# Performance work log

Measured on AMD Instinct MI355X. Metric: run time of the kernel, lower is better.

Reference implementation:

```python
import jax, jax.numpy as jnp
import numpy as np

B, S, CL, DIM, HEADS, FFN = 2, 2048, 512, 2048, 16, 8192
EPS = 1e-6


def rms_norm(x, w):
    return x * jax.lax.rsqrt(jnp.mean(x * x, axis=-1, keepdims=True) + EPS) * w


def mha(q, k, v, num_heads):
    b, sq, d = q.shape
    sk = k.shape[1]
    hd = d // num_heads
    q = q.reshape(b, sq, num_heads, hd)
    k = k.reshape(b, sk, num_heads, hd)
    v = v.reshape(b, sk, num_heads, hd)
    attn = jnp.einsum('bqhd,bkhd->bhqk', q, k) * (hd ** -0.5)
    attn = jax.nn.softmax(attn, axis=-1)
    out = jnp.einsum('bhqk,bkhd->bqhd', attn, v)
    return out.reshape(b, sq, d)


def setup_inputs() -> dict:
    key = jax.random.key(0)
    ks = iter(jax.random.split(key, 48))
    nrm = lambda shape, scale: jax.random.normal(next(ks), shape, jnp.float32) * scale
    w_scale = DIM ** -0.5
    inp = {
        'x': nrm((B, S, DIM), 1.0),
        'e': nrm((B, 6, DIM), 0.5),
        'context': nrm((B, CL, DIM), 1.0),
        'modulation': nrm((1, 6, DIM), w_scale),
        'norm1_w': jnp.ones((DIM,), jnp.float32),
        'norm2_w': jnp.ones((DIM,), jnp.float32),
        'norm3_w': jnp.ones((DIM,), jnp.float32),
        'sa_nq_w': jnp.ones((DIM,), jnp.float32),
        'sa_nk_w': jnp.ones((DIM,), jnp.float32),
        'ffn_norm_w': jnp.ones((DIM,), jnp.float32),
        'sa_qw': nrm((DIM, DIM), w_scale), 'sa_qb': jnp.zeros((DIM,), jnp.float32),
        'sa_kw': nrm((DIM, DIM), w_scale), 'sa_kb': jnp.zeros((DIM,), jnp.float32),
        'sa_vw': nrm((DIM, DIM), w_scale), 'sa_vb': jnp.zeros((DIM,), jnp.float32),
        'sa_ow': nrm((DIM, DIM), w_scale), 'sa_ob': jnp.zeros((DIM,), jnp.float32),
        'ca_qw': nrm((DIM, DIM), w_scale), 'ca_qb': jnp.zeros((DIM,), jnp.float32),
        'ca_kw': nrm((DIM, DIM), w_scale), 'ca_kb': jnp.zeros((DIM,), jnp.float32),
        'ca_vw': nrm((DIM, DIM), w_scale), 'ca_vb': jnp.zeros((DIM,), jnp.float32),
        'ca_ow': nrm((DIM, DIM), w_scale), 'ca_ob': jnp.zeros((DIM,), jnp.float32),
        'ffn_w1': nrm((DIM, FFN), w_scale), 'ffn_b1': jnp.zeros((FFN,), jnp.float32),
        'ffn_w2': nrm((FFN, DIM), FFN ** -0.5), 'ffn_b2': jnp.zeros((DIM,), jnp.float32),
    }
    return inp


def reference(x, e, context, modulation, norm1_w, norm2_w, norm3_w, sa_nq_w, sa_nk_w,
              ffn_norm_w, sa_qw, sa_qb, sa_kw, sa_kb, sa_vw, sa_vb, sa_ow, sa_ob,
              ca_qw, ca_qb, ca_kw, ca_kb, ca_vw, ca_vb, ca_ow, ca_ob,
              ffn_w1, ffn_b1, ffn_w2, ffn_b2):
    # AdaLN modulation: (modulation + e) chunked into 6 along dim=1 -> each [B,1,DIM]
    mod = modulation + e
    e0, e1, e2, e3, e4, e5 = [mod[:, i:i + 1, :] for i in range(6)]

    # --- self attention with qk_norm=True ---
    h = rms_norm(x, norm1_w) * (1.0 + e1) + e0
    q = rms_norm(h @ sa_qw + sa_qb, sa_nq_w)
    k = rms_norm(h @ sa_kw + sa_kb, sa_nk_w)
    v = h @ sa_vw + sa_vb
    y = mha(q, k, v, HEADS) @ sa_ow + sa_ob
    x = x + y * e2

    # --- cross attention (cross_attn_norm=False, no qk norm) ---
    h = rms_norm(x, norm2_w)
    q = h @ ca_qw + ca_qb
    k = context @ ca_kw + ca_kb
    v = context @ ca_vw + ca_vb
    y = mha(q, k, v, HEADS) @ ca_ow + ca_ob
    x = x + y

    # --- FFN: modulate(norm3(x)) -> RMSNorm -> Linear -> GELU(tanh) -> Linear ---
    h = rms_norm(x, norm3_w) * (1.0 + e4) + e3
    h = rms_norm(h, ffn_norm_w)
    h = jax.nn.gelu(h @ ffn_w1 + ffn_b1, approximate=True)
    y = h @ ffn_w2 + ffn_b2
    x = x + y * e5
    return x
```

## Files before the change

### kernel.cpp

```cpp
#include <hip/hip_runtime.h>
#include <hip/hip_bf16.h>
#include <cstdint>

#define DIM   2048
#define HEADS 16
#define HD    128
#define SEQ   2048
#define CLEN  512
#define FFND  8192
#define BATCH 2

using bf16 = __hip_bfloat16;
typedef __attribute__((ext_vector_type(8))) short  short8;
typedef __attribute__((ext_vector_type(4))) short  short4v;
typedef __attribute__((ext_vector_type(4))) float  f32x4;
typedef __attribute__((ext_vector_type(8))) __bf16 bf16x8;

__device__ __forceinline__ short f2bs(float f){ bf16 h = __float2bfloat16(f); return __builtin_bit_cast(short, h); }
__device__ __forceinline__ float bs2f(short s){ return __builtin_bit_cast(float, (uint32_t)((uint16_t)s) << 16); }

__device__ __forceinline__ f32x4 mfma16(short8 a, short8 b, f32x4 c){
  return __builtin_amdgcn_mfma_f32_16x16x32_bf16(
      __builtin_bit_cast(bf16x8, a), __builtin_bit_cast(bf16x8, b), c, 0, 0, 0);
}

__device__ __forceinline__ void gload_lds16(const void* g, const void* l){
  __builtin_amdgcn_global_load_lds(
      (const __attribute__((address_space(1))) void*)(uintptr_t)g,
      (__attribute__((address_space(3))) void*)(uint32_t)(uintptr_t)l, 16, 0, 0);
}

__device__ __forceinline__ float block_sum(float v, float* sbuf, int tid){
  #pragma unroll
  for (int m = 32; m >= 1; m >>= 1) v += __shfl_xor(v, m, 64);
  const int w = tid >> 6;
  if ((tid & 63) == 0) sbuf[w] = v;
  __syncthreads();
  float r = sbuf[0] + sbuf[1] + sbuf[2] + sbuf[3];
  __syncthreads();
  return r;
}


__global__ void modadd_k(const float* __restrict__ m, const float* __restrict__ e,
                         float* __restrict__ out){
  int i = blockIdx.x * 256 + threadIdx.x;
  out[i] = m[i % (6 * DIM)] + e[i];
}

__global__ void f2b8_k(const float* __restrict__ in, bf16* __restrict__ out){
  int i = blockIdx.x * 256 + threadIdx.x;
  const float4* p = (const float4*)in;
  float4 a = p[2*i], c = p[2*i+1];
  short8 o;
  o[0]=f2bs(a.x); o[1]=f2bs(a.y); o[2]=f2bs(a.z); o[3]=f2bs(a.w);
  o[4]=f2bs(c.x); o[5]=f2bs(c.y); o[6]=f2bs(c.z); o[7]=f2bs(c.w);
  *((short8*)out + i) = o;
}

__global__ __launch_bounds__(256) void transpose_w(const float* __restrict__ W,
                                                   bf16* __restrict__ Wt, int K, int N){
  __shared__ float tile[32][33];
  const int tx = threadIdx.x & 31, ty = threadIdx.x >> 5;
  const size_t k0 = blockIdx.y * 32, n0 = blockIdx.x * 32;
  #pragma unroll
  for (int i = 0; i < 4; i++)
    tile[ty + i*8][tx] = W[(k0 + ty + i*8) * (size_t)N + n0 + tx];
  __syncthreads();
  #pragma unroll
  for (int i = 0; i < 4; i++)
    Wt[(n0 + ty + i*8) * (size_t)K + k0 + tx] = __float2bfloat16(tile[tx][ty + i*8]);
}

template<int MODE>
__global__ __launch_bounds__(256) void norm_x(const float* __restrict__ x,
    const float* __restrict__ w1, const float* __restrict__ w2,
    const float* __restrict__ mod, bf16* __restrict__ out, int S)
{
  const int row = blockIdx.x, tid = threadIdx.x;
  const int b = row / S;
  __shared__ float sbuf[4];
  const float* xr = x + (size_t)row * DIM;
  float v[8];
  #pragma unroll
  for (int i = 0; i < 2; i++){
    float4 t = *(const float4*)(xr + i*1024 + tid*4);
    v[i*4+0]=t.x; v[i*4+1]=t.y; v[i*4+2]=t.z; v[i*4+3]=t.w;
  }
  float ss = 0.f;
  #pragma unroll
  for (int j = 0; j < 8; j++) ss += v[j]*v[j];
  ss = block_sum(ss, sbuf, tid);
  const float r = rsqrtf(ss * (1.0f/DIM) + 1e-6f);
  const float* mb = mod + (size_t)b * 6 * DIM;
  float t8[8];
  #pragma unroll
  for (int i = 0; i < 2; i++)
    #pragma unroll
    for (int j = 0; j < 4; j++){
      int n = i*1024 + tid*4 + j;
      float val = v[i*4+j] * r * w1[n];
      if (MODE == 1) val = val * (1.f + mb[DIM + n]) + mb[n];
      if (MODE == 3) val = val * (1.f + mb[4*DIM + n]) + mb[3*DIM + n];
      t8[i*4+j] = val;
    }
  if (MODE == 3){
    float s2 = 0.f;
    #pragma unroll
    for (int j = 0; j < 8; j++) s2 += t8[j]*t8[j];
    s2 = block_sum(s2, sbuf, tid);
    const float r2 = rsqrtf(s2 * (1.0f/DIM) + 1e-6f);
    #pragma unroll
    for (int i = 0; i < 2; i++)
      #pragma unroll
      for (int j = 0; j < 4; j++){
        int n = i*1024 + tid*4 + j;
        t8[i*4+j] = t8[i*4+j] * r2 * w2[n];
      }
  }
  #pragma unroll
  for (int i = 0; i < 2; i++){
    short4v o;
    #pragma unroll
    for (int j = 0; j < 4; j++) o[j] = f2bs(t8[i*4+j]);
    *(short4v*)(out + (size_t)row*DIM + i*1024 + tid*4) = o;
  }
}

__global__ __launch_bounds__(256) void rmsnorm_bf16_ip(bf16* __restrict__ x,
                                                       const float* __restrict__ w){
  const int row = blockIdx.x, tid = threadIdx.x;
  __shared__ float sbuf[4];
  bf16* xr = x + (size_t)row * DIM;
  short8 v = *(const short8*)(xr + tid*8);
  float f[8]; float ss = 0.f;
  #pragma unroll
  for (int j = 0; j < 8; j++){ f[j] = bs2f(v[j]); ss += f[j]*f[j]; }
  ss = block_sum(ss, sbuf, tid);
  const float r = rsqrtf(ss * (1.0f/DIM) + 1e-6f);
  short8 o;
  #pragma unroll
  for (int j = 0; j < 8; j++) o[j] = f2bs(f[j] * r * w[tid*8 + j]);
  *(short8*)(xr + tid*8) = o;
}

#define GBUF 24576
template<int EPI>
__global__ __launch_bounds__(512, 2) void gemm_bf16(
    const bf16* __restrict__ A, const bf16* __restrict__ Bt,
    const float* __restrict__ bias, const float* __restrict__ xin,
    const float* __restrict__ mod, float* __restrict__ outf,
    bf16* __restrict__ outb, int M, int N, int K, int S_tok, int eidx)
{
  __shared__ __align__(16) char lds[3][GBUF];
  const int tid = threadIdx.x;
  const int w = tid >> 6, l = tid & 63;
  const int lrow = l & 15, lhi = l >> 4;
  const int wm = w >> 2, wn = w & 3;
  const size_t m0 = (size_t)blockIdx.y * 128, n0 = (size_t)blockIdx.x * 256;

  f32x4 acc[4][4] = {};

  auto gofs = [&](int sid){ return (size_t)(sid >> 2) * K + (size_t)(((sid & 3) ^ ((sid >> 3) & 3)) * 8); };
  const bf16* gA0 = A  + m0 * K + gofs(tid);
  const bf16* gB0 = Bt + n0 * K + gofs(tid);
  const bf16* gB1 = Bt + n0 * K + gofs(tid + 512);

  auto stage = [&](int kt, char* buf){
    const size_t ko = (size_t)kt * 32;
    gload_lds16(gA0 + ko, buf + tid * 16);
    gload_lds16(gB0 + ko, buf + 8192 + tid * 16);
    gload_lds16(gB1 + ko, buf + 8192 + (tid + 512) * 16);
  };

  const int nt = K >> 5;
  stage(0, lds[0]);
  stage(1, lds[1]);
  asm volatile("s_waitcnt vmcnt(3)" ::: "memory");
  __builtin_amdgcn_s_barrier();
  __builtin_amdgcn_sched_barrier(0);

  const int sread = (lhi ^ ((lrow >> 1) & 3)) * 16;

  int bi = 0;
  for (int t = 0; t < nt; ++t){
    const char* br = lds[bi];
    const bool st = (t + 2 < nt);
    if (st){
      int wi = bi + 2; if (wi >= 3) wi -= 3;
      stage(t + 2, lds[wi]);
    }
    short8 af[4], bf[4];
    #pragma unroll
    for (int mi = 0; mi < 4; mi++)
      af[mi] = *(const short8*)(br + (wm*64 + mi*16 + lrow)*64 + sread);
    #pragma unroll
    for (int ni = 0; ni < 4; ni++)
      bf[ni] = *(const short8*)(br + 8192 + (wn*64 + ni*16 + lrow)*64 + sread);
    __builtin_amdgcn_s_setprio(1);
    #pragma unroll
    for (int mi = 0; mi < 4; mi++)
      #pragma unroll
      for (int ni = 0; ni < 4; ni++)
        acc[mi][ni] = mfma16(af[mi], bf[ni], acc[mi][ni]);
    __builtin_amdgcn_s_setprio(0);
    if (st)               { asm volatile("s_waitcnt vmcnt(3)" ::: "memory"); }
    else if (t + 1 < nt)  { asm volatile("s_waitcnt vmcnt(0)" ::: "memory"); }
    __builtin_amdgcn_s_barrier();
    __builtin_amdgcn_sched_barrier(0);
    bi = (bi + 1 == 3) ? 0 : bi + 1;
  }

  #pragma unroll
  for (int mi = 0; mi < 4; mi++)
    #pragma unroll
    for (int ni = 0; ni < 4; ni++)
      #pragma unroll
      for (int r = 0; r < 4; r++){
        const size_t m = m0 + wm*64 + mi*16 + lhi*4 + r;
        const size_t n = n0 + wn*64 + ni*16 + lrow;
        float v = acc[mi][ni][r] + bias[n];
        if constexpr (EPI == 0) {
          outb[m * N + n] = __float2bfloat16(v);
        } else if constexpr (EPI == 1) {
          const size_t b = m / S_tok, s = m % S_tok;
          const size_t h = n >> 7, d = n & 127;
          outb[((b*HEADS + h)*HD + d) * S_tok + s] = __float2bfloat16(v);
        } else if constexpr (EPI == 2) {
          const float ev = mod[(m / S_tok) * 6 * DIM + (size_t)eidx * DIM + n];
          outf[m * N + n] = xin[m * N + n] + v * ev;
        } else if constexpr (EPI == 3) {
          outf[m * N + n] += v;
        } else {
          float u = 0.7978845608028654f * (v + 0.044715f * v * v * v);
          outb[m * N + n] = __float2bfloat16(0.5f * v * (1.0f + tanhf(u)));
        }
      }
}

__global__ __launch_bounds__(256, 2) void attn_fwd(
    const bf16* __restrict__ Q, const bf16* __restrict__ Kp, const bf16* __restrict__ Vt,
    bf16* __restrict__ O, int SQ, int SKV)
{
  const int tid = threadIdx.x, w = tid >> 6, l = tid & 63;
  const int lrow = l & 15, lhi = l >> 4;
  const int nwg = gridDim.x;
  const int p = blockIdx.x;
  const int f = (p & 7) * (nwg >> 3) + (p >> 3);
  const int nqb = SQ >> 6;
  const int xq = f % nqb;
  const int h  = (f / nqb) % HEADS;
  const int b  = f / (nqb * HEADS);
  const int q0 = xq * 64 + w * 16;

  __shared__ __align__(16) char kls[2][16384];
  __shared__ __align__(16) char vls[2][16384];
  __shared__ __align__(16) bf16 P[4][16][72];
  const float scale = 0.08838834764831845f;

  const bf16* qp = Q + ((size_t)(b*SQ + q0 + lrow))*DIM + h*HD + lhi*8;
  short8 qf[4];
  #pragma unroll
  for (int ds = 0; ds < 4; ds++) qf[ds] = *(const short8*)(qp + ds*32);

  const bf16* kg = Kp + (size_t)b*SKV*DIM + h*HD;
  const bf16* vg = Vt + (size_t)(b*HEADS + h)*HD*SKV;

  f32x4 acc[8] = {};
  float m_run = -INFINITY, l_run = 0.f;
  const int nt = SKV >> 6;

  auto stage = [&](int buf, int kv0){
    char* kd = &kls[buf][0];
    #pragma unroll
    for (int i = 0; i < 4; i++){
      int sid = i*256 + tid;
      int row = sid >> 4, sg = sid & 15;
      int gsg = sg ^ (row & 7);
      gload_lds16(kg + (size_t)(kv0 + row)*DIM + gsg*8, kd + sid*16);
    }
    char* vd = &vls[buf][0];
    #pragma unroll
    for (int i = 0; i < 4; i++){
      int sid = i*256 + tid;
      int d = sid >> 3, sg = sid & 7;
      int gsg = sg ^ (d & 7);
      gload_lds16(vg + (size_t)d*SKV + kv0 + gsg*8, vd + sid*16);
    }
  };

  stage(0, 0);
  __syncthreads();

  for (int t = 0; t < nt; ++t){
    if (t + 1 < nt) stage((t + 1) & 1, (t + 1) * 64);
    const char* kb = &kls[t & 1][0];
    const char* vb = &vls[t & 1][0];

    f32x4 st[4] = {};
    #pragma unroll
    for (int kvf = 0; kvf < 4; kvf++){
      const int row = kvf*16 + lrow;
      const int rx = row & 7;
      #pragma unroll
      for (int ds = 0; ds < 4; ds++){
        const int seg = (ds*4 + lhi) ^ rx;
        short8 kf = *(const short8*)(kb + row*256 + seg*16);
        st[kvf] = mfma16(kf, qf[ds], st[kvf]);
      }
    }

    float sv[16]; float smax = -INFINITY;
    #pragma unroll
    for (int kvf = 0; kvf < 4; kvf++)
      #pragma unroll
      for (int r = 0; r < 4; r++){
        float xv = st[kvf][r] * scale;
        sv[kvf*4+r] = xv; smax = fmaxf(smax, xv);
      }
    smax = fmaxf(smax, __shfl_xor(smax, 16, 64));
    smax = fmaxf(smax, __shfl_xor(smax, 32, 64));
    const float mnew = fmaxf(m_run, smax);
    const float corr = __expf(m_run - mnew);
    float psum = 0.f;
    #pragma unroll
    for (int i = 0; i < 16; i++){ float pe = __expf(sv[i] - mnew); sv[i] = pe; psum += pe; }
    psum += __shfl_xor(psum, 16, 64); psum += __shfl_xor(psum, 32, 64);
    l_run = l_run * corr + psum;
    m_run = mnew;

    #pragma unroll
    for (int kvf = 0; kvf < 4; kvf++){
      short4v o;
      #pragma unroll
      for (int r = 0; r < 4; r++) o[r] = f2bs(sv[kvf*4+r]);
      *(short4v*)&P[w][lrow][kvf*16 + lhi*4] = o;
    }

    float cr[4];
    #pragma unroll
    for (int r = 0; r < 4; r++) cr[r] = __shfl(corr, lhi*4 + r, 64);
    #pragma unroll
    for (int df = 0; df < 8; df++){
      acc[df][0] *= cr[0]; acc[df][1] *= cr[1]; acc[df][2] *= cr[2]; acc[df][3] *= cr[3];
    }

    asm volatile("s_waitcnt lgkmcnt(0)" ::: "memory");
    __builtin_amdgcn_sched_barrier(0);

    short8 pf0 = *(const short8*)&P[w][lrow][lhi*8];
    short8 pf1 = *(const short8*)&P[w][lrow][32 + lhi*8];
    #pragma unroll
    for (int df = 0; df < 8; df++){
      const int d = df*16 + lrow;
      const int dx = d & 7;
      short8 vf0 = *(const short8*)(vb + d*128 + ((lhi)     ^ dx)*16);
      short8 vf1 = *(const short8*)(vb + d*128 + ((lhi + 4) ^ dx)*16);
      acc[df] = mfma16(pf0, vf0, acc[df]);
      acc[df] = mfma16(pf1, vf1, acc[df]);
    }
    __syncthreads();
  }

  const float linv = 1.0f / l_run;
  float li[4];
  #pragma unroll
  for (int r = 0; r < 4; r++) li[r] = __shfl(linv, lhi*4 + r, 64);
  #pragma unroll
  for (int df = 0; df < 8; df++)
    #pragma unroll
    for (int r = 0; r < 4; r++){
      const size_t q = q0 + lhi*4 + r;
      O[((size_t)(b*SQ + q))*DIM + h*HD + df*16 + lrow] = __float2bfloat16(acc[df][r] * li[r]);
    }
}


extern "C" void kernel_launch(void* const* d_in, const int* in_sizes, int n_in,
                              void* d_out, int out_size, void* d_ws, size_t ws_size,
                              hipStream_t stream)
{
  const float* x    = (const float*)d_in[0];
  const float* e    = (const float*)d_in[1];
  const float* ctx  = (const float*)d_in[2];
  const float* modw = (const float*)d_in[3];
  const float* n1w  = (const float*)d_in[4];
  const float* n2w  = (const float*)d_in[5];
  const float* n3w  = (const float*)d_in[6];
  const float* nqw  = (const float*)d_in[7];
  const float* nkw  = (const float*)d_in[8];
  const float* fnw  = (const float*)d_in[9];
  const float* saqw = (const float*)d_in[10]; const float* saqb = (const float*)d_in[11];
  const float* sakw = (const float*)d_in[12]; const float* sakb = (const float*)d_in[13];
  const float* savw = (const float*)d_in[14]; const float* savb = (const float*)d_in[15];
  const float* saow = (const float*)d_in[16]; const float* saob = (const float*)d_in[17];
  const float* caqw = (const float*)d_in[18]; const float* caqb = (const float*)d_in[19];
  const float* cakw = (const float*)d_in[20]; const float* cakb = (const float*)d_in[21];
  const float* cavw = (const float*)d_in[22]; const float* cavb = (const float*)d_in[23];
  const float* caow = (const float*)d_in[24]; const float* caob = (const float*)d_in[25];
  const float* fw1  = (const float*)d_in[26]; const float* fb1  = (const float*)d_in[27];
  const float* fw2  = (const float*)d_in[28]; const float* fb2  = (const float*)d_in[29];
  float* out = (float*)d_out;
  (void)in_sizes; (void)n_in; (void)out_size; (void)ws_size;

  char* ws = (char*)d_ws;
  size_t off = 0;
  auto alloc = [&](size_t bytes) -> void* {
    void* p = ws + off; off = (off + bytes + 255) & ~(size_t)255; return p;
  };
  bf16*  wt   = (bf16*)alloc((size_t)FFND * DIM * 2);
  float* mod  = (float*)alloc((size_t)BATCH * 6 * DIM * 4);
  bf16*  ctxb = (bf16*)alloc((size_t)BATCH * CLEN * DIM * 2);
  bf16*  hbuf = (bf16*)alloc((size_t)BATCH * SEQ * DIM * 2);
  bf16*  qbuf = (bf16*)alloc((size_t)BATCH * SEQ * DIM * 2);
  bf16*  kbuf = (bf16*)alloc((size_t)BATCH * SEQ * DIM * 2);
  bf16*  vtb  = (bf16*)alloc((size_t)BATCH * SEQ * DIM * 2);
  bf16*  aout = (bf16*)alloc((size_t)BATCH * SEQ * DIM * 2);
  float* xcur = (float*)alloc((size_t)BATCH * SEQ * DIM * 4);
  bf16*  hf   = (bf16*)alloc((size_t)BATCH * SEQ * FFND * 2);

  const int M = BATCH * SEQ;
  const int Mc = BATCH * CLEN;

  modadd_k<<<dim3(96), dim3(256), 0, stream>>>(modw, e, mod);
  f2b8_k<<<dim3(1024), dim3(256), 0, stream>>>(ctx, ctxb);

  norm_x<1><<<dim3(M), dim3(256), 0, stream>>>(x, n1w, nullptr, mod, hbuf, SEQ);

  transpose_w<<<dim3(DIM/32, DIM/32), dim3(256), 0, stream>>>(saqw, wt, DIM, DIM);
  gemm_bf16<0><<<dim3(DIM/256, M/128), dim3(512), 0, stream>>>(hbuf, wt, saqb, nullptr, mod, nullptr, qbuf, M, DIM, DIM, SEQ, 0);
  rmsnorm_bf16_ip<<<dim3(M), dim3(256), 0, stream>>>(qbuf, nqw);

  transpose_w<<<dim3(DIM/32, DIM/32), dim3(256), 0, stream>>>(sakw, wt, DIM, DIM);
  gemm_bf16<0><<<dim3(DIM/256, M/128), dim3(512), 0, stream>>>(hbuf, wt, sakb, nullptr, mod, nullptr, kbuf, M, DIM, DIM, SEQ, 0);
  rmsnorm_bf16_ip<<<dim3(M), dim3(256), 0, stream>>>(kbuf, nkw);

  transpose_w<<<dim3(DIM/32, DIM/32), dim3(256), 0, stream>>>(savw, wt, DIM, DIM);
  gemm_bf16<1><<<dim3(DIM/256, M/128), dim3(512), 0, stream>>>(hbuf, wt, savb, nullptr, mod, nullptr, vtb, M, DIM, DIM, SEQ, 0);

  attn_fwd<<<dim3((SEQ/64)*HEADS*BATCH), dim3(256), 0, stream>>>(qbuf, kbuf, vtb, aout, SEQ, SEQ);

  transpose_w<<<dim3(DIM/32, DIM/32), dim3(256), 0, stream>>>(saow, wt, DIM, DIM);
  gemm_bf16<2><<<dim3(DIM/256, M/128), dim3(512), 0, stream>>>(aout, wt, saob, x, mod, xcur, nullptr, M, DIM, DIM, SEQ, 2);

  norm_x<2><<<dim3(M), dim3(256), 0, stream>>>(xcur, n2w, nullptr, mod, hbuf, SEQ);

  transpose_w<<<dim3(DIM/32, DIM/32), dim3(256), 0, stream>>>(caqw, wt, DIM, DIM);
  gemm_bf16<0><<<dim3(DIM/256, M/128), dim3(512), 0, stream>>>(hbuf, wt, caqb, nullptr, mod, nullptr, qbuf, M, DIM, DIM, SEQ, 0);

  transpose_w<<<dim3(DIM/32, DIM/32), dim3(256), 0, stream>>>(cakw, wt, DIM, DIM);
  gemm_bf16<0><<<dim3(DIM/256, Mc/128), dim3(512), 0, stream>>>(ctxb, wt, cakb, nullptr, mod, nullptr, kbuf, Mc, DIM, DIM, CLEN, 0);

  transpose_w<<<dim3(DIM/32, DIM/32), dim3(256), 0, stream>>>(cavw, wt, DIM, DIM);
  gemm_bf16<1><<<dim3(DIM/256, Mc/128), dim3(512), 0, stream>>>(ctxb, wt, cavb, nullptr, mod, nullptr, vtb, Mc, DIM, DIM, CLEN, 0);

  attn_fwd<<<dim3((SEQ/64)*HEADS*BATCH), dim3(256), 0, stream>>>(qbuf, kbuf, vtb, aout, SEQ, CLEN);

  transpose_w<<<dim3(DIM/32, DIM/32), dim3(256), 0, stream>>>(caow, wt, DIM, DIM);
  gemm_bf16<3><<<dim3(DIM/256, M/128), dim3(512), 0, stream>>>(aout, wt, caob, nullptr, mod, xcur, nullptr, M, DIM, DIM, SEQ, 0);

  norm_x<3><<<dim3(M), dim3(256), 0, stream>>>(xcur, n3w, fnw, mod, hbuf, SEQ);

  transpose_w<<<dim3(FFND/32, DIM/32), dim3(256), 0, stream>>>(fw1, wt, DIM, FFND);
  gemm_bf16<4><<<dim3(FFND/256, M/128), dim3(512), 0, stream>>>(hbuf, wt, fb1, nullptr, mod, nullptr, hf, M, FFND, DIM, SEQ, 0);

  transpose_w<<<dim3(DIM/32, FFND/32), dim3(256), 0, stream>>>(fw2, wt, FFND, DIM);
  gemm_bf16<2><<<dim3(DIM/256, M/128), dim3(512), 0, stream>>>(hf, wt, fb2, xcur, mod, out, nullptr, M, DIM, FFND, SEQ, 5);
}
```

Baseline: 948.9 us.

## Deepen GEMM LDS pipeline to four stages, prefetch A fragments, remap blocks across XCDs

```diff
diff --git a/kernel.cpp b/kernel.cpp
--- a/kernel.cpp
+++ b/kernel.cpp
@@ -152,12 +152,16 @@
     const float* __restrict__ mod, float* __restrict__ outf,
     bf16* __restrict__ outb, int M, int N, int K, int S_tok, int eidx)
 {
-  __shared__ __align__(16) char lds[3][GBUF];
+  __shared__ __align__(16) char lds[4][GBUF];
   const int tid = threadIdx.x;
   const int w = tid >> 6, l = tid & 63;
   const int lrow = l & 15, lhi = l >> 4;
   const int wm = w >> 2, wn = w & 3;
-  const size_t m0 = (size_t)blockIdx.y * 128, n0 = (size_t)blockIdx.x * 256;
+  const int q = gridDim.x >> 3;
+  const int f = ((int)blockIdx.x & 7) * q + ((int)blockIdx.x >> 3);
+  const int Mt = M >> 7;
+  const size_t m0 = (size_t)(f % Mt) * 128;
+  const size_t n0 = (size_t)(f / Mt) * 256;
 
   f32x4 acc[4][4] = {};
 
@@ -176,24 +180,23 @@
   const int nt = K >> 5;
   stage(0, lds[0]);
   stage(1, lds[1]);
+  stage(2, lds[2]);
   asm volatile("s_waitcnt vmcnt(3)" ::: "memory");
   __builtin_amdgcn_s_barrier();
-  __builtin_amdgcn_sched_barrier(0);
 
   const int sread = (lhi ^ ((lrow >> 1) & 3)) * 16;
 
-  int bi = 0;
+  short8 pf[4];
+  #pragma unroll
+  for (int mi = 0; mi < 4; mi++)
+    pf[mi] = *(const short8*)(lds[0] + (wm*64 + mi*16 + lrow)*64 + sread);
+
   for (int t = 0; t < nt; ++t){
-    const char* br = lds[bi];
-    const bool st = (t + 2 < nt);
-    if (st){
-      int wi = bi + 2; if (wi >= 3) wi -= 3;
-      stage(t + 2, lds[wi]);
-    }
+    const char* br = lds[t & 3];
+    if (t + 3 < nt) stage(t + 3, lds[(t + 3) & 3]);
     short8 af[4], bf[4];
     #pragma unroll
-    for (int mi = 0; mi < 4; mi++)
-      af[mi] = *(const short8*)(br + (wm*64 + mi*16 + lrow)*64 + sread);
+    for (int mi = 0; mi < 4; mi++) af[mi] = pf[mi];
     #pragma unroll
     for (int ni = 0; ni < 4; ni++)
       bf[ni] = *(const short8*)(br + 8192 + (wn*64 + ni*16 + lrow)*64 + sread);
@@ -204,11 +207,15 @@
       for (int ni = 0; ni < 4; ni++)
         acc[mi][ni] = mfma16(af[mi], bf[ni], acc[mi][ni]);
     __builtin_amdgcn_s_setprio(0);
-    if (st)               { asm volatile("s_waitcnt vmcnt(3)" ::: "memory"); }
-    else if (t + 1 < nt)  { asm volatile("s_waitcnt vmcnt(0)" ::: "memory"); }
+    if (t + 1 < nt){
+      const char* nb = lds[(t + 1) & 3];
+      #pragma unroll
+      for (int mi = 0; mi < 4; mi++)
+        pf[mi] = *(const short8*)(nb + (wm*64 + mi*16 + lrow)*64 + sread);
+    }
+    if (t + 3 < nt) { asm volatile("s_waitcnt vmcnt(3)" ::: "memory"); }
+    else            { asm volatile("s_waitcnt vmcnt(0)" ::: "memory"); }
     __builtin_amdgcn_s_barrier();
-    __builtin_amdgcn_sched_barrier(0);
-    bi = (bi + 1 == 3) ? 0 : bi + 1;
   }
 
   #pragma unroll
@@ -428,42 +435,42 @@
   norm_x<1><<<dim3(M), dim3(256), 0, stream>>>(x, n1w, nullptr, mod, hbuf, SEQ);
 
   transpose_w<<<dim3(DIM/32, DIM/32), dim3(256), 0, stream>>>(saqw, wt, DIM, DIM);
-  gemm_bf16<0><<<dim3(DIM/256, M/128), dim3(512), 0, stream>>>(hbuf, wt, saqb, nullptr, mod, nullptr, qbuf, M, DIM, DIM, SEQ, 0);
+  gemm_bf16<0><<<dim3((M/128)*(DIM/256)), dim3(512), 0, stream>>>(hbuf, wt, saqb, nullptr, mod, nullptr, qbuf, M, DIM, DIM, SEQ, 0);
   rmsnorm_bf16_ip<<<dim3(M), dim3(256), 0, stream>>>(qbuf, nqw);
 
   transpose_w<<<dim3(DIM/32, DIM/32), dim3(256), 0, stream>>>(sakw, wt, DIM, DIM);
-  gemm_bf16<0><<<dim3(DIM/256, M/128), dim3(512), 0, stream>>>(hbuf, wt, sakb, nullptr, mod, nullptr, kbuf, M, DIM, DIM, SEQ, 0);
+  gemm_bf16<0><<<dim3((M/128)*(DIM/256)), dim3(512), 0, stream>>>(hbuf, wt, sakb, nullptr, mod, nullptr, kbuf, M, DIM, DIM, SEQ, 0);
   rmsnorm_bf16_ip<<<dim3(M), dim3(256), 0, stream>>>(kbuf, nkw);
 
   transpose_w<<<dim3(DIM/32, DIM/32), dim3(256), 0, stream>>>(savw, wt, DIM, DIM);
-  gemm_bf16<1><<<dim3(DIM/256, M/128), dim3(512), 0, stream>>>(hbuf, wt, savb, nullptr, mod, nullptr, vtb, M, DIM, DIM, SEQ, 0);
+  gemm_bf16<1><<<dim3((M/128)*(DIM/256)), dim3(512), 0, stream>>>(hbuf, wt, savb, nullptr, mod, nullptr, vtb, M, DIM, DIM, SEQ, 0);
 
   attn_fwd<<<dim3((SEQ/64)*HEADS*BATCH), dim3(256), 0, stream>>>(qbuf, kbuf, vtb, aout, SEQ, SEQ);
 
   transpose_w<<<dim3(DIM/32, DIM/32), dim3(256), 0, stream>>>(saow, wt, DIM, DIM);
-  gemm_bf16<2><<<dim3(DIM/256, M/128), dim3(512), 0, stream>>>(aout, wt, saob, x, mod, xcur, nullptr, M, DIM, DIM, SEQ, 2);
+  gemm_bf16<2><<<dim3((M/128)*(DIM/256)), dim3(512), 0, stream>>>(aout, wt, saob, x, mod, xcur, nullptr, M, DIM, DIM, SEQ, 2);
 
   norm_x<2><<<dim3(M), dim3(256), 0, stream>>>(xcur, n2w, nullptr, mod, hbuf, SEQ);
 
   transpose_w<<<dim3(DIM/32, DIM/32), dim3(256), 0, stream>>>(caqw, wt, DIM, DIM);
-  gemm_bf16<0><<<dim3(DIM/256, M/128), dim3(512), 0, stream>>>(hbuf, wt, caqb, nullptr, mod, nullptr, qbuf, M, DIM, DIM, SEQ, 0);
+  gemm_bf16<0><<<dim3((M/128)*(DIM/256)), dim3(512), 0, stream>>>(hbuf, wt, caqb, nullptr, mod, nullptr, qbuf, M, DIM, DIM, SEQ, 0);
 
   transpose_w<<<dim3(DIM/32, DIM/32), dim3(256), 0, stream>>>(cakw, wt, DIM, DIM);
-  gemm_bf16<0><<<dim3(DIM/256, Mc/128), dim3(512), 0, stream>>>(ctxb, wt, cakb, nullptr, mod, nullptr, kbuf, Mc, DIM, DIM, CLEN, 0);
+  gemm_bf16<0><<<dim3((Mc/128)*(DIM/256)), dim3(512), 0, stream>>>(ctxb, wt, cakb, nullptr, mod, nullptr, kbuf, Mc, DIM, DIM, CLEN, 0);
 
   transpose_w<<<dim3(DIM/32, DIM/32), dim3(256), 0, stream>>>(cavw, wt, DIM, DIM);
-  gemm_bf16<1><<<dim3(DIM/256, Mc/128), dim3(512), 0, stream>>>(ctxb, wt, cavb, nullptr, mod, nullptr, vtb, Mc, DIM, DIM, CLEN, 0);
+  gemm_bf16<1><<<dim3((Mc/128)*(DIM/256)), dim3(512), 0, stream>>>(ctxb, wt, cavb, nullptr, mod, nullptr, vtb, Mc, DIM, DIM, CLEN, 0);
 
   attn_fwd<<<dim3((SEQ/64)*HEADS*BATCH), dim3(256), 0, stream>>>(qbuf, kbuf, vtb, aout, SEQ, CLEN);
 
   transpose_w<<<dim3(DIM/32, DIM/32), dim3(256), 0, stream>>>(caow, wt, DIM, DIM);
-  gemm_bf16<3><<<dim3(DIM/256, M/128), dim3(512), 0, stream>>>(aout, wt, caob, nullptr, mod, xcur, nullptr, M, DIM, DIM, SEQ, 0);
+  gemm_bf16<3><<<dim3((M/128)*(DIM/256)), dim3(512), 0, stream>>>(aout, wt, caob, nullptr, mod, xcur, nullptr, M, DIM, DIM, SEQ, 0);
 
   norm_x<3><<<dim3(M), dim3(256), 0, stream>>>(xcur, n3w, fnw, mod, hbuf, SEQ);
 
   transpose_w<<<dim3(FFND/32, DIM/32), dim3(256), 0, stream>>>(fw1, wt, DIM, FFND);
-  gemm_bf16<4><<<dim3(FFND/256, M/128), dim3(512), 0, stream>>>(hbuf, wt, fb1, nullptr, mod, nullptr, hf, M, FFND, DIM, SEQ, 0);
+  gemm_bf16<4><<<dim3((M/128)*(FFND/256)), dim3(512), 0, stream>>>(hbuf, wt, fb1, nullptr, mod, nullptr, hf, M, FFND, DIM, SEQ, 0);
 
   transpose_w<<<dim3(DIM/32, FFND/32), dim3(256), 0, stream>>>(fw2, wt, FFND, DIM);
-  gemm_bf16<2><<<dim3(DIM/256, M/128), dim3(512), 0, stream>>>(hf, wt, fb2, xcur, mod, out, nullptr, M, DIM, FFND, SEQ, 5);
-}
+  gemm_bf16<2><<<dim3((M/128)*(DIM/256)), dim3(512), 0, stream>>>(hf, wt, fb2, xcur, mod, out, nullptr, M, DIM, FFND, SEQ, 5);
+}
```

Result: slower. 973.9 us (+2.6%).

## Fuse QKV projections into one GEMM and add 256x256-tile GEMM kernel

Applied to the files above, without the earlier changes.

```diff
diff --git a/kernel.cpp b/kernel.cpp
--- a/kernel.cpp
+++ b/kernel.cpp
@@ -56,6 +56,13 @@
   o[0]=f2bs(a.x); o[1]=f2bs(a.y); o[2]=f2bs(a.z); o[3]=f2bs(a.w);
   o[4]=f2bs(c.x); o[5]=f2bs(c.y); o[6]=f2bs(c.z); o[7]=f2bs(c.w);
   *((short8*)out + i) = o;
+}
+
+__global__ void biascat_k(const float* __restrict__ b0, const float* __restrict__ b1,
+                          const float* __restrict__ b2, float* __restrict__ bcat){
+  int i = blockIdx.x * 256 + threadIdx.x;
+  const float* src = (i < DIM) ? b0 : (i < 2*DIM) ? b1 : b2;
+  bcat[i] = src[i & (DIM-1)];
 }
 
 __global__ __launch_bounds__(256) void transpose_w(const float* __restrict__ W,
@@ -234,6 +241,100 @@
         } else {
           float u = 0.7978845608028654f * (v + 0.044715f * v * v * v);
           outb[m * N + n] = __float2bfloat16(0.5f * v * (1.0f + tanhf(u)));
+        }
+      }
+}
+
+#define GBUF2 32768
+template<int EPI>
+__global__ __launch_bounds__(512, 2) void gemm_big(
+    const bf16* __restrict__ A, const bf16* __restrict__ Bt,
+    const float* __restrict__ bias, bf16* __restrict__ out0,
+    bf16* __restrict__ out1, bf16* __restrict__ out2,
+    int M, int N, int K, int S_tok)
+{
+  __shared__ __align__(16) char lds[3][GBUF2];
+  const int tid = threadIdx.x;
+  const int w = tid >> 6, l = tid & 63;
+  const int lrow = l & 15, lhi = l >> 4;
+  const int wr = w >> 2, wc = w & 3;
+  const size_t m0 = (size_t)blockIdx.y * 256, n0 = (size_t)blockIdx.x * 256;
+
+  f32x4 acc[8][4] = {};
+
+  auto gofs = [&](int sid){ return (size_t)(sid >> 2) * K + (size_t)(((sid & 3) ^ ((sid >> 3) & 3)) * 8); };
+  const bf16* gA0 = A  + m0 * K + gofs(tid);
+  const bf16* gA1 = A  + m0 * K + gofs(tid + 512);
+  const bf16* gB0 = Bt + n0 * K + gofs(tid);
+  const bf16* gB1 = Bt + n0 * K + gofs(tid + 512);
+
+  auto stage = [&](int kt, char* buf){
+    const size_t ko = (size_t)kt * 32;
+    gload_lds16(gA0 + ko, buf + tid * 16);
+    gload_lds16(gA1 + ko, buf + (tid + 512) * 16);
+    gload_lds16(gB0 + ko, buf + 16384 + tid * 16);
+    gload_lds16(gB1 + ko, buf + 16384 + (tid + 512) * 16);
+  };
+
+  const int nt = K >> 5;
+  stage(0, lds[0]);
+  stage(1, lds[1]);
+  asm volatile("s_waitcnt vmcnt(4)" ::: "memory");
+  __builtin_amdgcn_s_barrier();
+  __builtin_amdgcn_sched_barrier(0);
+
+  const int sread = (lhi ^ ((lrow >> 1) & 3)) * 16;
+
+  int bi = 0;
+  for (int t = 0; t < nt; ++t){
+    const char* br = lds[bi];
+    const bool st = (t + 2 < nt);
+    if (st){
+      int wi = bi + 2; if (wi >= 3) wi -= 3;
+      stage(t + 2, lds[wi]);
+    }
+    short8 af[8], bf[4];
+    #pragma unroll
+    for (int mi = 0; mi < 8; mi++)
+      af[mi] = *(const short8*)(br + (wr*128 + mi*16 + lrow)*64 + sread);
+    #pragma unroll
+    for (int ni = 0; ni < 4; ni++)
+      bf[ni] = *(const short8*)(br + 16384 + (wc*64 + ni*16 + lrow)*64 + sread);
+    __builtin_amdgcn_s_setprio(1);
+    #pragma unroll
+    for (int mi = 0; mi < 8; mi++)
+      #pragma unroll
+      for (int ni = 0; ni < 4; ni++)
+        acc[mi][ni] = mfma16(af[mi], bf[ni], acc[mi][ni]);
+    __builtin_amdgcn_s_setprio(0);
+    if (st)               { asm volatile("s_waitcnt vmcnt(4)" ::: "memory"); }
+    else if (t + 1 < nt)  { asm volatile("s_waitcnt vmcnt(0)" ::: "memory"); }
+    __builtin_amdgcn_s_barrier();
+    __builtin_amdgcn_sched_barrier(0);
+    bi = (bi + 1 == 3) ? 0 : bi + 1;
+  }
+
+  #pragma unroll
+  for (int mi = 0; mi < 8; mi++)
+    #pragma unroll
+    for (int ni = 0; ni < 4; ni++)
+      #pragma unroll
+      for (int r = 0; r < 4; r++){
+        const size_t m = m0 + wr*128 + mi*16 + lhi*4 + r;
+        const size_t n = n0 + wc*64 + ni*16 + lrow;
+        float v = acc[mi][ni][r] + bias[n];
+        if constexpr (EPI == 4) {
+          float u = 0.7978845608028654f * (v + 0.044715f * v * v * v);
+          out0[m * N + n] = __float2bfloat16(0.5f * v * (1.0f + tanhf(u)));
+        } else {
+          const size_t seg = n >> 11, col = n & 2047;
+          if (seg == 0)      out0[m * DIM + col] = __float2bfloat16(v);
+          else if (seg == 1) out1[m * DIM + col] = __float2bfloat16(v);
+          else {
+            const size_t b = m / S_tok, s = m % S_tok;
+            const size_t h = col >> 7, d = col & 127;
+            out2[((b*HEADS + h)*HD + d) * S_tok + s] = __float2bfloat16(v);
+          }
         }
       }
 }
@@ -410,6 +511,7 @@
   };
   bf16*  wt   = (bf16*)alloc((size_t)FFND * DIM * 2);
   float* mod  = (float*)alloc((size_t)BATCH * 6 * DIM * 4);
+  float* bcat = (float*)alloc((size_t)3 * DIM * 4);
   bf16*  ctxb = (bf16*)alloc((size_t)BATCH * CLEN * DIM * 2);
   bf16*  hbuf = (bf16*)alloc((size_t)BATCH * SEQ * DIM * 2);
   bf16*  qbuf = (bf16*)alloc((size_t)BATCH * SEQ * DIM * 2);
@@ -424,19 +526,16 @@
 
   modadd_k<<<dim3(96), dim3(256), 0, stream>>>(modw, e, mod);
   f2b8_k<<<dim3(1024), dim3(256), 0, stream>>>(ctx, ctxb);
+  biascat_k<<<dim3(24), dim3(256), 0, stream>>>(saqb, sakb, savb, bcat);
 
   norm_x<1><<<dim3(M), dim3(256), 0, stream>>>(x, n1w, nullptr, mod, hbuf, SEQ);
 
-  transpose_w<<<dim3(DIM/32, DIM/32), dim3(256), 0, stream>>>(saqw, wt, DIM, DIM);
-  gemm_bf16<0><<<dim3(DIM/256, M/128), dim3(512), 0, stream>>>(hbuf, wt, saqb, nullptr, mod, nullptr, qbuf, M, DIM, DIM, SEQ, 0);
+  transpose_w<<<dim3(DIM/32, DIM/32), dim3(256), 0, stream>>>(saqw, wt,                          DIM, DIM);
+  transpose_w<<<dim3(DIM/32, DIM/32), dim3(256), 0, stream>>>(sakw, wt + (size_t)DIM*DIM,        DIM, DIM);
+  transpose_w<<<dim3(DIM/32, DIM/32), dim3(256), 0, stream>>>(savw, wt + (size_t)2*DIM*DIM,      DIM, DIM);
+  gemm_big<5><<<dim3(3*DIM/256, M/256), dim3(512), 0, stream>>>(hbuf, wt, bcat, qbuf, kbuf, vtb, M, 3*DIM, DIM, SEQ);
   rmsnorm_bf16_ip<<<dim3(M), dim3(256), 0, stream>>>(qbuf, nqw);
-
-  transpose_w<<<dim3(DIM/32, DIM/32), dim3(256), 0, stream>>>(sakw, wt, DIM, DIM);
-  gemm_bf16<0><<<dim3(DIM/256, M/128), dim3(512), 0, stream>>>(hbuf, wt, sakb, nullptr, mod, nullptr, kbuf, M, DIM, DIM, SEQ, 0);
   rmsnorm_bf16_ip<<<dim3(M), dim3(256), 0, stream>>>(kbuf, nkw);
-
-  transpose_w<<<dim3(DIM/32, DIM/32), dim3(256), 0, stream>>>(savw, wt, DIM, DIM);
-  gemm_bf16<1><<<dim3(DIM/256, M/128), dim3(512), 0, stream>>>(hbuf, wt, savb, nullptr, mod, nullptr, vtb, M, DIM, DIM, SEQ, 0);
 
   attn_fwd<<<dim3((SEQ/64)*HEADS*BATCH), dim3(256), 0, stream>>>(qbuf, kbuf, vtb, aout, SEQ, SEQ);
 
@@ -462,7 +561,7 @@
   norm_x<3><<<dim3(M), dim3(256), 0, stream>>>(xcur, n3w, fnw, mod, hbuf, SEQ);
 
   transpose_w<<<dim3(FFND/32, DIM/32), dim3(256), 0, stream>>>(fw1, wt, DIM, FFND);
-  gemm_bf16<4><<<dim3(FFND/256, M/128), dim3(512), 0, stream>>>(hbuf, wt, fb1, nullptr, mod, nullptr, hf, M, FFND, DIM, SEQ, 0);
+  gemm_big<4><<<dim3(FFND/256, M/256), dim3(512), 0, stream>>>(hbuf, wt, fb1, hf, nullptr, nullptr, M, FFND, DIM, SEQ);
 
   transpose_w<<<dim3(DIM/32, FFND/32), dim3(256), 0, stream>>>(fw2, wt, FFND, DIM);
   gemm_bf16<2><<<dim3(DIM/256, M/128), dim3(512), 0, stream>>>(hf, wt, fb2, xcur, mod, out, nullptr, M, DIM, FFND, SEQ, 5);
```

Result: slower. 994.3 us (+4.8%).

## Fuse self-attention QKV projections into one GEMM and shrink GEMM tile to 128x128

Applied to the files above, without the earlier changes.

```diff
diff --git a/kernel.cpp b/kernel.cpp
--- a/kernel.cpp
+++ b/kernel.cpp
@@ -56,6 +56,13 @@
   o[0]=f2bs(a.x); o[1]=f2bs(a.y); o[2]=f2bs(a.z); o[3]=f2bs(a.w);
   o[4]=f2bs(c.x); o[5]=f2bs(c.y); o[6]=f2bs(c.z); o[7]=f2bs(c.w);
   *((short8*)out + i) = o;
+}
+
+__global__ void biascat_k(const float* __restrict__ b0, const float* __restrict__ b1,
+                          const float* __restrict__ b2, float* __restrict__ bcat){
+  int i = blockIdx.x * 256 + threadIdx.x;
+  const float* src = (i < DIM) ? b0 : (i < 2*DIM) ? b1 : b2;
+  bcat[i] = src[i & (DIM-1)];
 }
 
 __global__ __launch_bounds__(256) void transpose_w(const float* __restrict__ W,
@@ -144,39 +151,42 @@
   *(short8*)(xr + tid*8) = o;
 }
 
-#define GBUF 24576
+#define GBUF 16384
 template<int EPI>
-__global__ __launch_bounds__(512, 2) void gemm_bf16(
+__global__ __launch_bounds__(256, 2) void gemm_v12(
     const bf16* __restrict__ A, const bf16* __restrict__ Bt,
     const float* __restrict__ bias, const float* __restrict__ xin,
     const float* __restrict__ mod, float* __restrict__ outf,
-    bf16* __restrict__ outb, int M, int N, int K, int S_tok, int eidx)
+    bf16* __restrict__ outb, bf16* __restrict__ out1, bf16* __restrict__ out2,
+    int M, int N, int K, int S_tok, int eidx)
 {
   __shared__ __align__(16) char lds[3][GBUF];
   const int tid = threadIdx.x;
   const int w = tid >> 6, l = tid & 63;
   const int lrow = l & 15, lhi = l >> 4;
-  const int wm = w >> 2, wn = w & 3;
-  const size_t m0 = (size_t)blockIdx.y * 128, n0 = (size_t)blockIdx.x * 256;
+  const int wm = w >> 1, wn = w & 1;
+  const size_t m0 = (size_t)blockIdx.y * 128, n0 = (size_t)blockIdx.x * 128;
 
   f32x4 acc[4][4] = {};
 
-  auto gofs = [&](int sid){ return (size_t)(sid >> 2) * K + (size_t)(((sid & 3) ^ ((sid >> 3) & 3)) * 8); };
+  auto gofs = [&](int s){ return (size_t)(s >> 2) * K + (size_t)(((s & 3) ^ ((s >> 3) & 3)) * 8); };
   const bf16* gA0 = A  + m0 * K + gofs(tid);
+  const bf16* gA1 = A  + m0 * K + gofs(tid + 256);
   const bf16* gB0 = Bt + n0 * K + gofs(tid);
-  const bf16* gB1 = Bt + n0 * K + gofs(tid + 512);
+  const bf16* gB1 = Bt + n0 * K + gofs(tid + 256);
 
   auto stage = [&](int kt, char* buf){
     const size_t ko = (size_t)kt * 32;
     gload_lds16(gA0 + ko, buf + tid * 16);
+    gload_lds16(gA1 + ko, buf + (tid + 256) * 16);
     gload_lds16(gB0 + ko, buf + 8192 + tid * 16);
-    gload_lds16(gB1 + ko, buf + 8192 + (tid + 512) * 16);
+    gload_lds16(gB1 + ko, buf + 8192 + (tid + 256) * 16);
   };
 
   const int nt = K >> 5;
   stage(0, lds[0]);
   stage(1, lds[1]);
-  asm volatile("s_waitcnt vmcnt(3)" ::: "memory");
+  asm volatile("s_waitcnt vmcnt(4)" ::: "memory");
   __builtin_amdgcn_s_barrier();
   __builtin_amdgcn_sched_barrier(0);
 
@@ -204,7 +214,7 @@
       for (int ni = 0; ni < 4; ni++)
         acc[mi][ni] = mfma16(af[mi], bf[ni], acc[mi][ni]);
     __builtin_amdgcn_s_setprio(0);
-    if (st)               { asm volatile("s_waitcnt vmcnt(3)" ::: "memory"); }
+    if (st)               { asm volatile("s_waitcnt vmcnt(4)" ::: "memory"); }
     else if (t + 1 < nt)  { asm volatile("s_waitcnt vmcnt(0)" ::: "memory"); }
     __builtin_amdgcn_s_barrier();
     __builtin_amdgcn_sched_barrier(0);
@@ -231,9 +241,18 @@
           outf[m * N + n] = xin[m * N + n] + v * ev;
         } else if constexpr (EPI == 3) {
           outf[m * N + n] += v;
-        } else {
+        } else if constexpr (EPI == 4) {
           float u = 0.7978845608028654f * (v + 0.044715f * v * v * v);
           outb[m * N + n] = __float2bfloat16(0.5f * v * (1.0f + tanhf(u)));
+        } else {
+          const size_t sg = n >> 11, col = n & 2047;
+          if (sg == 0)      outb[m * DIM + col] = __float2bfloat16(v);
+          else if (sg == 1) out1[m * DIM + col] = __float2bfloat16(v);
+          else {
+            const size_t b = m / S_tok, s = m % S_tok;
+            const size_t h = col >> 7, d = col & 127;
+            out2[((b*HEADS + h)*HD + d) * S_tok + s] = __float2bfloat16(v);
+          }
         }
       }
 }
@@ -410,6 +429,7 @@
   };
   bf16*  wt   = (bf16*)alloc((size_t)FFND * DIM * 2);
   float* mod  = (float*)alloc((size_t)BATCH * 6 * DIM * 4);
+  float* bcat = (float*)alloc((size_t)3 * DIM * 4);
   bf16*  ctxb = (bf16*)alloc((size_t)BATCH * CLEN * DIM * 2);
   bf16*  hbuf = (bf16*)alloc((size_t)BATCH * SEQ * DIM * 2);
   bf16*  qbuf = (bf16*)alloc((size_t)BATCH * SEQ * DIM * 2);
@@ -424,46 +444,43 @@
 
   modadd_k<<<dim3(96), dim3(256), 0, stream>>>(modw, e, mod);
   f2b8_k<<<dim3(1024), dim3(256), 0, stream>>>(ctx, ctxb);
+  biascat_k<<<dim3(24), dim3(256), 0, stream>>>(saqb, sakb, savb, bcat);
 
   norm_x<1><<<dim3(M), dim3(256), 0, stream>>>(x, n1w, nullptr, mod, hbuf, SEQ);
 
-  transpose_w<<<dim3(DIM/32, DIM/32), dim3(256), 0, stream>>>(saqw, wt, DIM, DIM);
-  gemm_bf16<0><<<dim3(DIM/256, M/128), dim3(512), 0, stream>>>(hbuf, wt, saqb, nullptr, mod, nullptr, qbuf, M, DIM, DIM, SEQ, 0);
+  transpose_w<<<dim3(DIM/32, DIM/32), dim3(256), 0, stream>>>(saqw, wt,                     DIM, DIM);
+  transpose_w<<<dim3(DIM/32, DIM/32), dim3(256), 0, stream>>>(sakw, wt + (size_t)DIM*DIM,   DIM, DIM);
+  transpose_w<<<dim3(DIM/32, DIM/32), dim3(256), 0, stream>>>(savw, wt + (size_t)2*DIM*DIM, DIM, DIM);
+  gemm_v12<5><<<dim3(3*DIM/128, M/128), dim3(256), 0, stream>>>(hbuf, wt, bcat, nullptr, nullptr, nullptr, qbuf, kbuf, vtb, M, 3*DIM, DIM, SEQ, 0);
   rmsnorm_bf16_ip<<<dim3(M), dim3(256), 0, stream>>>(qbuf, nqw);
-
-  transpose_w<<<dim3(DIM/32, DIM/32), dim3(256), 0, stream>>>(sakw, wt, DIM, DIM);
-  gemm_bf16<0><<<dim3(DIM/256, M/128), dim3(512), 0, stream>>>(hbuf, wt, sakb, nullptr, mod, nullptr, kbuf, M, DIM, DIM, SEQ, 0);
   rmsnorm_bf16_ip<<<dim3(M), dim3(256), 0, stream>>>(kbuf, nkw);
 
-  transpose_w<<<dim3(DIM/32, DIM/32), dim3(256), 0, stream>>>(savw, wt, DIM, DIM);
-  gemm_bf16<1><<<dim3(DIM/256, M/128), dim3(512), 0, stream>>>(hbuf, wt, savb, nullptr, mod, nullptr, vtb, M, DIM, DIM, SEQ, 0);
-
   attn_fwd<<<dim3((SEQ/64)*HEADS*BATCH), dim3(256), 0, stream>>>(qbuf, kbuf, vtb, aout, SEQ, SEQ);
 
   transpose_w<<<dim3(DIM/32, DIM/32), dim3(256), 0, stream>>>(saow, wt, DIM, DIM);
-  gemm_bf16<2><<<dim3(DIM/256, M/128), dim3(512), 0, stream>>>(aout, wt, saob, x, mod, xcur, nullptr, M, DIM, DIM, SEQ, 2);
+  gemm_v12<2><<<dim3(DIM/128, M/128), dim3(256), 0, stream>>>(aout, wt, saob, x, mod, xcur, nullptr, nullptr, nullptr, M, DIM, DIM, SEQ, 2);
 
   norm_x<2><<<dim3(M), dim3(256), 0, stream>>>(xcur, n2w, nullptr, mod, hbuf, SEQ);
 
   transpose_w<<<dim3(DIM/32, DIM/32), dim3(256), 0, stream>>>(caqw, wt, DIM, DIM);
-  gemm_bf16<0><<<dim3(DIM/256, M/128), dim3(512), 0, stream>>>(hbuf, wt, caqb, nullptr, mod, nullptr, qbuf, M, DIM, DIM, SEQ, 0);
+  gemm_v12<0><<<dim3(DIM/128, M/128), dim3(256), 0, stream>>>(hbuf, wt, caqb, nullptr, nullptr, nullptr, qbuf, nullptr, nullptr, M, DIM, DIM, SEQ, 0);
 
   transpose_w<<<dim3(DIM/32, DIM/32), dim3(256), 0, stream>>>(cakw, wt, DIM, DIM);
-  gemm_bf16<0><<<dim3(DIM/256, Mc/128), dim3(512), 0, stream>>>(ctxb, wt, cakb, nullptr, mod, nullptr, kbuf, Mc, DIM, DIM, CLEN, 0);
+  gemm_v12<0><<<dim3(DIM/128, Mc/128), dim3(256), 0, stream>>>(ctxb, wt, cakb, nullptr, nullptr, nullptr, kbuf, nullptr, nullptr, Mc, DIM, DIM, CLEN, 0);
 
   transpose_w<<<dim3(DIM/32, DIM/32), dim3(256), 0, stream>>>(cavw, wt, DIM, DIM);
-  gemm_bf16<1><<<dim3(DIM/256, Mc/128), dim3(512), 0, stream>>>(ctxb, wt, cavb, nullptr, mod, nullptr, vtb, Mc, DIM, DIM, CLEN, 0);
+  gemm_v12<1><<<dim3(DIM/128, Mc/128), dim3(256), 0, stream>>>(ctxb, wt, cavb, nullptr, nullptr, nullptr, vtb, nullptr, nullptr, Mc, DIM, DIM, CLEN, 0);
 
   attn_fwd<<<dim3((SEQ/64)*HEADS*BATCH), dim3(256), 0, stream>>>(qbuf, kbuf, vtb, aout, SEQ, CLEN);
 
   transpose_w<<<dim3(DIM/32, DIM/32), dim3(256), 0, stream>>>(caow, wt, DIM, DIM);
-  gemm_bf16<3><<<dim3(DIM/256, M/128), dim3(512), 0, stream>>>(aout, wt, caob, nullptr, mod, xcur, nullptr, M, DIM, DIM, SEQ, 0);
+  gemm_v12<3><<<dim3(DIM/128, M/128), dim3(256), 0, stream>>>(aout, wt, caob, nullptr, nullptr, xcur, nullptr, nullptr, nullptr, M, DIM, DIM, SEQ, 0);
 
   norm_x<3><<<dim3(M), dim3(256), 0, stream>>>(xcur, n3w, fnw, mod, hbuf, SEQ);
 
   transpose_w<<<dim3(FFND/32, DIM/32), dim3(256), 0, stream>>>(fw1, wt, DIM, FFND);
-  gemm_bf16<4><<<dim3(FFND/256, M/128), dim3(512), 0, stream>>>(hbuf, wt, fb1, nullptr, mod, nullptr, hf, M, FFND, DIM, SEQ, 0);
+  gemm_v12<4><<<dim3(FFND/128, M/128), dim3(256), 0, stream>>>(hbuf, wt, fb1, nullptr, nullptr, nullptr, hf, nullptr, nullptr, M, FFND, DIM, SEQ, 0);
 
   transpose_w<<<dim3(DIM/32, FFND/32), dim3(256), 0, stream>>>(fw2, wt, FFND, DIM);
-  gemm_bf16<2><<<dim3(DIM/256, M/128), dim3(512), 0, stream>>>(hf, wt, fb2, xcur, mod, out, nullptr, M, DIM, FFND, SEQ, 5);
-}
+  gemm_v12<2><<<dim3(DIM/128, M/128), dim3(256), 0, stream>>>(hf, wt, fb2, xcur, mod, out, nullptr, nullptr, nullptr, M, DIM, FFND, SEQ, 5);
+}
```

Measured after the change: 990.7 us. 1.04x slower.
